# Performance work log

Measured on AMD Instinct MI355X. Metric: run time of the kernel, lower is better.

## Reference

```python
import jax, jax.numpy as jnp
import numpy as np


def setup_inputs() -> dict:
    key = jax.random.key(0)
    ks = jax.random.split(key, 6)
    B, C, H, W = 8, 1024, 48, 48
    K = 32            # keep_topk
    Cg = C // K       # channels per group = 32
    return {
        "corr_features": jax.random.normal(ks[0], (B, H, W, H, W), jnp.float32),
        "cur_features": jax.random.normal(ks[1], (B, C, H, W), jnp.float32),
        "ref_mask": jax.random.uniform(ks[2], (B, 1, 384, 384), dtype=jnp.float32),
        # grouped 1x1 conv: per-group weight [K, out_per_group, in_per_group]
        "group_w": jax.random.normal(ks[3], (K, Cg, Cg), jnp.float32) * 0.02,
        "group_b": jnp.zeros((C,), jnp.float32),
        # global 1x1 conv: [out=Cg, in=C]
        "global_w": jax.random.normal(ks[4], (Cg, C), jnp.float32) * 0.02,
        "global_b": jnp.zeros((Cg,), jnp.float32),
    }


def reference(corr_features, cur_features, ref_mask, group_w, group_b, global_w, global_b):
    B, ch, cw, rh, rw = corr_features.shape
    C = cur_features.shape[1]
    K, Cg, _ = group_w.shape  # K = keep_topk, Cg = C // K

    cur_flat = cur_features.reshape(B, C, ch * cw)          # [B,C,N]
    corr = corr_features.reshape(B, ch * cw, rh * rw)       # [B,N,M]

    # F.interpolate(..., mode='bilinear', align_corners=False) == half-pixel linear resize
    mask = jax.image.resize(ref_mask, (B, 1, rh, rw), method="linear")
    mask = (mask.reshape(B, 1, rh * rw) > 0.5).astype(jnp.float32)
    fg_corr = corr * mask                                    # [B,N,M]

    # get_struct_info: topk over summed correlation, gather channel features
    scores = fg_corr.sum(axis=-1)                            # [B,N]
    _, idx = jax.lax.top_k(scores, K)                        # [B,K]
    struct = jnp.take_along_axis(cur_flat, idx[:, None, :], axis=2)  # [B,C,K]
    struct = jnp.swapaxes(struct, 1, 2)                      # [B,K,C]

    # bmm(struct, cur_flat): [B,K,C] x [B,C,N] -> [B,K,N]
    struct_info = jnp.einsum('bkc,bcn->bkn', struct, cur_flat).reshape(B, K, ch, cw)

    # grouped 1x1 conv (groups=K) + ReLU
    xg = cur_features.reshape(B, K, Cg, ch, cw)
    group_feat = jnp.einsum('bkihw,koi->bkohw', xg, group_w)
    group_feat = jax.nn.relu(group_feat + group_b.reshape(K, Cg)[None, :, :, None, None])

    # repeat struct_info across each group's Cg channels, multiply, sum over groups
    group_struct = (struct_info[:, :, None, :, :] * group_feat).sum(axis=1)  # [B,Cg,H,W]

    # global 1x1 conv + ReLU
    global_feat = jnp.einsum('bchw,oc->bohw', cur_features, global_w)
    global_feat = jax.nn.relu(global_feat + global_b[None, :, None, None])   # [B,Cg,H,W]
    global_struct = struct_info.mean(axis=1, keepdims=True) * global_feat

    return jnp.concatenate([group_struct, global_struct], axis=1)  # [B,2*Cg,H,W]
```

## Files before the change

### kernel.cpp

```cpp
#include <hip/hip_runtime.h>
#include <math.h>

#define BB 8
#define CC 1024
#define HW 48
#define NN 2304
#define MM 2304
#define KK 32

typedef __attribute__((ext_vector_type(8))) short short8v;
typedef __attribute__((ext_vector_type(4))) float f32x4;

__device__ __forceinline__ unsigned short f2bf(float f) {
    unsigned u = __float_as_uint(f);
    return (unsigned short)((u + 0x7FFFu + ((u >> 16) & 1u)) >> 16);
}

__device__ __forceinline__ void gll16(const unsigned short* g, unsigned short* l) {
    __builtin_amdgcn_global_load_lds(
        (const __attribute__((address_space(1))) void*)g,
        (__attribute__((address_space(3))) void*)l, 16, 0, 0);
}

__global__ void mask_kernel(const float* __restrict__ rm, float* __restrict__ mask) {
    int t = blockIdx.x * 256 + threadIdx.x;
    if (t >= BB * NN) return;
    int b = t / NN, p = t % NN;
    int y = p / HW, x = p % HW;
    const float* src = rm + (size_t)b * 384 * 384;

    int jx0 = 8 * x - 4;
    float wx[16];
    float wxs = 0.f;
    #pragma unroll
    for (int dx = 0; dx < 16; ++dx) {
        int jx = jx0 + dx;
        float w = 1.0f - fabsf((float)dx - 7.5f) * 0.125f;
        if (jx >= 0 && jx < 384) { wx[dx] = w; wxs += w; } else wx[dx] = 0.f;
    }
    int jy0 = 8 * y - 4;
    float acc = 0.f, wys = 0.f;
    for (int dy = 0; dy < 16; ++dy) {
        int jy = jy0 + dy;
        if (jy < 0 || jy >= 384) continue;
        float wy = 1.0f - fabsf((float)dy - 7.5f) * 0.125f;
        wys += wy;
        const float* row = src + (size_t)jy * 384;
        float rs = 0.f;
        #pragma unroll
        for (int dx = 0; dx < 16; ++dx) {
            if (wx[dx] > 0.f) rs += wx[dx] * row[jx0 + dx];
        }
        acc += wy * rs;
    }
    float v = acc / (wys * wxs);
    mask[t] = (v > 0.5f) ? 1.0f : 0.0f;
}

__global__ void scores_kernel(const float* __restrict__ corr, const float* __restrict__ mask,
                              float* __restrict__ scores) {
    int wave = threadIdx.x >> 6, lane = threadIdx.x & 63;
    int row = blockIdx.x * 4 + wave;
    int b = row / NN, n = row % NN;
    const float4* cr = (const float4*)(corr + ((size_t)b * NN + n) * MM);
    const float4* mr = (const float4*)(mask + (size_t)b * MM);
    float acc = 0.f;
    #pragma unroll
    for (int it = 0; it < 9; ++it) {
        int i = it * 64 + lane;
        float4 cv = cr[i];
        float4 mv = mr[i];
        acc += cv.x * mv.x + cv.y * mv.y + cv.z * mv.z + cv.w * mv.w;
    }
    #pragma unroll
    for (int off = 32; off >= 1; off >>= 1) acc += __shfl_down(acc, off);
    if (lane == 0) scores[row] = acc;
}

__global__ void topk1_kernel(const float* __restrict__ scores,
                             float* __restrict__ cval, int* __restrict__ cidx) {
    int b = blockIdx.x >> 3, ch = blockIdx.x & 7;
    int t = threadIdx.x;
    const float* s = scores + b * NN + ch * 288;
    float v0 = s[t];
    float v1 = (t < 32) ? s[256 + t] : -INFINITY;
    int i0 = t, i1 = 256 + t;
    __shared__ float wv[4]; __shared__ int wi[4];
    __shared__ float bwv; __shared__ int bwi;
    for (int it = 0; it < KK; ++it) {
        float bv = (v0 >= v1) ? v0 : v1;
        int   bi = (v0 >= v1) ? i0 : i1;
        #pragma unroll
        for (int off = 32; off >= 1; off >>= 1) {
            float ov = __shfl_down(bv, off);
            int   oi = __shfl_down(bi, off);
            if (ov > bv || (ov == bv && oi < bi)) { bv = ov; bi = oi; }
        }
        if ((t & 63) == 0) { wv[t >> 6] = bv; wi[t >> 6] = bi; }
        __syncthreads();
        if (t == 0) {
            #pragma unroll
            for (int u = 1; u < 4; ++u)
                if (wv[u] > bv || (wv[u] == bv && wi[u] < bi)) { bv = wv[u]; bi = wi[u]; }
            bwv = bv; bwi = bi;
            cval[(b * 8 + ch) * 32 + it] = bv;
            cidx[(b * 8 + ch) * 32 + it] = ch * 288 + bi;
        }
        __syncthreads();
        int W = bwi;
        if (i0 == W) v0 = -INFINITY;
        if (i1 == W) v1 = -INFINITY;
    }
}

__global__ void topk2_kernel(const float* __restrict__ cval, const int* __restrict__ cidx,
                             int* __restrict__ idxo) {
    int b = blockIdx.x, t = threadIdx.x;
    float v = cval[b * 256 + t];
    int gi = cidx[b * 256 + t];
    __shared__ float wv[4]; __shared__ int wi[4];
    __shared__ int bwi_s;
    for (int it = 0; it < KK; ++it) {
        float bv = v; int bi = gi;
        #pragma unroll
        for (int off = 32; off >= 1; off >>= 1) {
            float ov = __shfl_down(bv, off);
            int   oi = __shfl_down(bi, off);
            if (ov > bv || (ov == bv && oi < bi)) { bv = ov; bi = oi; }
        }
        if ((t & 63) == 0) { wv[t >> 6] = bv; wi[t >> 6] = bi; }
        __syncthreads();
        if (t == 0) {
            #pragma unroll
            for (int u = 1; u < 4; ++u)
                if (wv[u] > bv || (wv[u] == bv && wi[u] < bi)) { bv = wv[u]; bi = wi[u]; }
            idxo[b * KK + it] = bi;
            bwi_s = bi;
        }
        __syncthreads();
        if (gi == bwi_s) v = -INFINITY;
    }
}

__global__ void gather_kernel(const float* __restrict__ cur, const int* __restrict__ idx,
                              unsigned short* __restrict__ st) {
    int t = blockIdx.x * 256 + threadIdx.x;
    int c = t & (CC - 1); int bk = t >> 10; int k = bk & 31; int b = bk >> 5;
    int id = idx[b * KK + k];
    st[t] = f2bf(cur[((size_t)b * CC + c) * NN + id]);
}

__global__ void wconv_kernel(const float* __restrict__ gw, const float* __restrict__ glw,
                             unsigned short* __restrict__ gwh, unsigned short* __restrict__ glwh) {
    int t = blockIdx.x * 256 + threadIdx.x;
    gwh[t] = f2bf(gw[t]);
    glwh[t] = f2bf(glw[t]);
}

__global__ __launch_bounds__(256) void fused_mfma(
    const float* __restrict__ cur, const unsigned short* __restrict__ st16,
    const unsigned short* __restrict__ gwh, const unsigned short* __restrict__ glwh,
    const float* __restrict__ gb, const float* __restrict__ glb,
    float* __restrict__ out)
{
    __shared__ unsigned short XT[2][1024];
    __shared__ unsigned short AC[2][1024];
    __shared__ unsigned short GC[2][1024];
    __shared__ float SIL[32][33];
    __shared__ float GBL[CC];
    __shared__ float MS[32];
    __shared__ float GLBL[32];

    int blk = blockIdx.x;
    int b = blk / 72, n0 = (blk % 72) * 32;
    int t = threadIdx.x;
    int w = t >> 6, l = t & 63;
    int m = w >> 1, nt = w & 1;

    for (int i = t; i < CC; i += 256) GBL[i] = gb[i];
    if (t < 32) GLBL[t] = glb[t];

    const float* curb = cur + (size_t)b * CC * NN;
    const unsigned short* stb = st16 + b * (KK * CC);

    int ci = t >> 3, ns = t & 7;
    const float* xsrc0 = curb + (size_t)(2 * ci) * NN + n0 + 4 * ns;
    const float* xsrc1 = xsrc0 + NN;

    int fro = (16 * m + (l & 15)) * 32 + 8 * (l >> 4);
    int fxo = (16 * nt + (l & 15)) * 32 + 8 * (l >> 4);

    if (t < 128) {
        float4 f0 = *(const float4*)(xsrc0);
        float4 f1 = *(const float4*)(xsrc1);
        unsigned pk;
        pk = (unsigned)f2bf(f0.x) | ((unsigned)f2bf(f1.x) << 16); *(unsigned*)&XT[0][(4*ns+0)*32 + 2*ci] = pk;
        pk = (unsigned)f2bf(f0.y) | ((unsigned)f2bf(f1.y) << 16); *(unsigned*)&XT[0][(4*ns+1)*32 + 2*ci] = pk;
        pk = (unsigned)f2bf(f0.z) | ((unsigned)f2bf(f1.z) << 16); *(unsigned*)&XT[0][(4*ns+2)*32 + 2*ci] = pk;
        pk = (unsigned)f2bf(f0.w) | ((unsigned)f2bf(f1.w) << 16); *(unsigned*)&XT[0][(4*ns+3)*32 + 2*ci] = pk;
    } else if (w == 2) {
        gll16(stb + (l >> 2) * CC + (l & 3) * 8, &AC[0][0]);
        gll16(stb + (16 + (l >> 2)) * CC + (l & 3) * 8, &AC[0][512]);
    } else {
        gll16(glwh + (l >> 2) * CC + (l & 3) * 8, &GC[0][0]);
        gll16(glwh + (16 + (l >> 2)) * CC + (l & 3) * 8, &GC[0][512]);
    }
    __syncthreads();

    f32x4 siacc = {0.f, 0.f, 0.f, 0.f};
    f32x4 glacc = {0.f, 0.f, 0.f, 0.f};
    for (int cc = 0; cc < 32; ++cc) {
        int buf = cc & 1;
        bool stg = (cc < 31);
        float4 f0, f1;
        if (stg) {
            if (t < 128) {
                f0 = *(const float4*)(xsrc0 + (size_t)(cc + 1) * 32 * NN);
                f1 = *(const float4*)(xsrc1 + (size_t)(cc + 1) * 32 * NN);
            } else if (w == 2) {
                gll16(stb + (l >> 2) * CC + (cc + 1) * 32 + (l & 3) * 8, &AC[buf ^ 1][0]);
                gll16(stb + (16 + (l >> 2)) * CC + (cc + 1) * 32 + (l & 3) * 8, &AC[buf ^ 1][512]);
            } else {
                gll16(glwh + (l >> 2) * CC + (cc + 1) * 32 + (l & 3) * 8, &GC[buf ^ 1][0]);
                gll16(glwh + (16 + (l >> 2)) * CC + (cc + 1) * 32 + (l & 3) * 8, &GC[buf ^ 1][512]);
            }
        }
        short8v ast = *(const short8v*)&AC[buf][fro];
        short8v agl = *(const short8v*)&GC[buf][fro];
        short8v bx  = *(const short8v*)&XT[buf][fxo];
        siacc = __builtin_amdgcn_mfma_f32_16x16x32_bf16(ast, bx, siacc, 0, 0, 0);
        glacc = __builtin_amdgcn_mfma_f32_16x16x32_bf16(agl, bx, glacc, 0, 0, 0);
        if (stg && t < 128) {
            int bo = buf ^ 1;
            unsigned pk;
            pk = (unsigned)f2bf(f0.x) | ((unsigned)f2bf(f1.x) << 16); *(unsigned*)&XT[bo][(4*ns+0)*32 + 2*ci] = pk;
            pk = (unsigned)f2bf(f0.y) | ((unsigned)f2bf(f1.y) << 16); *(unsigned*)&XT[bo][(4*ns+1)*32 + 2*ci] = pk;
            pk = (unsigned)f2bf(f0.z) | ((unsigned)f2bf(f1.z) << 16); *(unsigned*)&XT[bo][(4*ns+2)*32 + 2*ci] = pk;
            pk = (unsigned)f2bf(f0.w) | ((unsigned)f2bf(f1.w) << 16); *(unsigned*)&XT[bo][(4*ns+3)*32 + 2*ci] = pk;
        }
        __syncthreads();
    }

    #pragma unroll
    for (int r = 0; r < 4; ++r)
        SIL[16 * m + 4 * (l >> 4) + r][16 * nt + (l & 15)] = siacc[r];
    __syncthreads();
    if (t < 32) {
        float s = 0.f;
        #pragma unroll
        for (int k = 0; k < 32; ++k) s += SIL[k][t];
        MS[t] = s * (1.0f / 32.0f);
    }

    if (t < 128) {
        float4 f0 = *(const float4*)(xsrc0);
        float4 f1 = *(const float4*)(xsrc1);
        unsigned pk;
        pk = (unsigned)f2bf(f0.x) | ((unsigned)f2bf(f1.x) << 16); *(unsigned*)&XT[0][(4*ns+0)*32 + 2*ci] = pk;
        pk = (unsigned)f2bf(f0.y) | ((unsigned)f2bf(f1.y) << 16); *(unsigned*)&XT[0][(4*ns+1)*32 + 2*ci] = pk;
        pk = (unsigned)f2bf(f0.z) | ((unsigned)f2bf(f1.z) << 16); *(unsigned*)&XT[0][(4*ns+2)*32 + 2*ci] = pk;
        pk = (unsigned)f2bf(f0.w) | ((unsigned)f2bf(f1.w) << 16); *(unsigned*)&XT[0][(4*ns+3)*32 + 2*ci] = pk;
    } else if (w == 2) {
        gll16(gwh + l * 8, &AC[0][0]);
        gll16(gwh + 512 + l * 8, &AC[0][512]);
    }
    __syncthreads();

    f32x4 accg = {0.f, 0.f, 0.f, 0.f};
    const f32x4 zz = {0.f, 0.f, 0.f, 0.f};
    for (int k = 0; k < 32; ++k) {
        int buf = k & 1;
        bool stg = (k < 31);
        float4 f0, f1;
        if (stg) {
            if (t < 128) {
                f0 = *(const float4*)(xsrc0 + (size_t)(k + 1) * 32 * NN);
                f1 = *(const float4*)(xsrc1 + (size_t)(k + 1) * 32 * NN);
            } else if (w == 2) {
                gll16(gwh + (k + 1) * 1024 + l * 8, &AC[buf ^ 1][0]);
                gll16(gwh + (k + 1) * 1024 + 512 + l * 8, &AC[buf ^ 1][512]);
            }
        }
        short8v aw = *(const short8v*)&AC[buf][fro];
        short8v bx = *(const short8v*)&XT[buf][fxo];
        f32x4 gf = __builtin_amdgcn_mfma_f32_16x16x32_bf16(aw, bx, zz, 0, 0, 0);
        float sik = SIL[k][16 * nt + (l & 15)];
        #pragma unroll
        for (int r = 0; r < 4; ++r) {
            int orow = 16 * m + 4 * (l >> 4) + r;
            accg[r] += sik * fmaxf(gf[r] + GBL[k * 32 + orow], 0.f);
        }
        if (stg && t < 128) {
            int bo = buf ^ 1;
            unsigned pk;
            pk = (unsigned)f2bf(f0.x) | ((unsigned)f2bf(f1.x) << 16); *(unsigned*)&XT[bo][(4*ns+0)*32 + 2*ci] = pk;
            pk = (unsigned)f2bf(f0.y) | ((unsigned)f2bf(f1.y) << 16); *(unsigned*)&XT[bo][(4*ns+1)*32 + 2*ci] = pk;
            pk = (unsigned)f2bf(f0.z) | ((unsigned)f2bf(f1.z) << 16); *(unsigned*)&XT[bo][(4*ns+2)*32 + 2*ci] = pk;
            pk = (unsigned)f2bf(f0.w) | ((unsigned)f2bf(f1.w) << 16); *(unsigned*)&XT[bo][(4*ns+3)*32 + 2*ci] = pk;
        }
        __syncthreads();
    }

    int col = 16 * nt + (l & 15);
    size_t ob = (size_t)b * 64 * NN + n0 + col;
    float msv = MS[col];
    #pragma unroll
    for (int r = 0; r < 4; ++r) {
        int orow = 16 * m + 4 * (l >> 4) + r;
        out[ob + (size_t)orow * NN] = accg[r];
        out[ob + (size_t)(32 + orow) * NN] = fmaxf(glacc[r] + GLBL[orow], 0.f) * msv;
    }
}

extern "C" void kernel_launch(void* const* d_in, const int* in_sizes, int n_in,
                              void* d_out, int out_size, void* d_ws, size_t ws_size,
                              hipStream_t stream) {
    const float* corr = (const float*)d_in[0];
    const float* cur  = (const float*)d_in[1];
    const float* rm   = (const float*)d_in[2];
    const float* gw   = (const float*)d_in[3];
    const float* gb   = (const float*)d_in[4];
    const float* glw  = (const float*)d_in[5];
    const float* glb  = (const float*)d_in[6];
    float* out = (float*)d_out;
    float* ws  = (float*)d_ws;

    float* mask   = ws;
    float* scores = mask + BB * MM;
    float* cval   = scores + BB * NN;
    int*   cidx   = (int*)(cval + 2048);
    int*   idx    = cidx + 2048;
    unsigned short* st16 = (unsigned short*)(idx + 256);
    unsigned short* gwh  = st16 + BB * KK * CC;
    unsigned short* glwh = gwh + 32768;

    mask_kernel<<<(BB * NN + 255) / 256, 256, 0, stream>>>(rm, mask);
    scores_kernel<<<BB * NN / 4, 256, 0, stream>>>(corr, mask, scores);
    topk1_kernel<<<BB * 8, 256, 0, stream>>>(scores, cval, cidx);
    topk2_kernel<<<BB, 256, 0, stream>>>(cval, cidx, idx);
    gather_kernel<<<BB * KK * CC / 256, 256, 0, stream>>>(cur, idx, st16);
    wconv_kernel<<<128, 256, 0, stream>>>(gw, glw, gwh, glwh);
    fused_mfma<<<BB * (NN / 32), 256, 0, stream>>>(cur, st16, gwh, glwh, gb, glb, out);
}
```

Measured before the change: 172.7 us.

## Stage full-channel X tile once in LDS and split group conv across waves

The fused MFMA kernel now uses 16-column tiles instead of 32 and loads all 1024 channels of the current-feature tile into LDS once, as bf16 with an XOR swizzle. This replaces the two separate streamed, double-buffered passes over the same data, which had a barrier on every step. The A operands (struct rows, global weights, group weights) are read straight from global memory, not staged through LDS. Each wave now covers 8 of the 32 groups, and the partial sums are reduced through LDS at the end. The grid doubles and LDS use grows to about 32KB per block, which may limit occupancy.

```diff
diff --git a/kernel.cpp b/kernel.cpp
--- a/kernel.cpp
+++ b/kernel.cpp
@@ -14,12 +14,6 @@
 __device__ __forceinline__ unsigned short f2bf(float f) {
     unsigned u = __float_as_uint(f);
     return (unsigned short)((u + 0x7FFFu + ((u >> 16) & 1u)) >> 16);
-}
-
-__device__ __forceinline__ void gll16(const unsigned short* g, unsigned short* l) {
-    __builtin_amdgcn_global_load_lds(
-        (const __attribute__((address_space(1))) void*)g,
-        (__attribute__((address_space(3))) void*)l, 16, 0, 0);
 }
 
 __global__ void mask_kernel(const float* __restrict__ rm, float* __restrict__ mask) {
@@ -86,7 +80,7 @@
     float v1 = (t < 32) ? s[256 + t] : -INFINITY;
     int i0 = t, i1 = 256 + t;
     __shared__ float wv[4]; __shared__ int wi[4];
-    __shared__ float bwv; __shared__ int bwi;
+    __shared__ int bwi;
     for (int it = 0; it < KK; ++it) {
         float bv = (v0 >= v1) ? v0 : v1;
         int   bi = (v0 >= v1) ? i0 : i1;
@@ -102,7 +96,7 @@
             #pragma unroll
             for (int u = 1; u < 4; ++u)
                 if (wv[u] > bv || (wv[u] == bv && wi[u] < bi)) { bv = wv[u]; bi = wi[u]; }
-            bwv = bv; bwi = bi;
+            bwi = bi;
             cval[(b * 8 + ch) * 32 + it] = bv;
             cidx[(b * 8 + ch) * 32 + it] = ch * 288 + bi;
         }
@@ -163,152 +157,106 @@
     const float* __restrict__ gb, const float* __restrict__ glb,
     float* __restrict__ out)
 {
-    __shared__ unsigned short XT[2][1024];
-    __shared__ unsigned short AC[2][1024];
-    __shared__ unsigned short GC[2][1024];
-    __shared__ float SIL[32][33];
+    __shared__ unsigned short XT[16 * 1024];
+    __shared__ float SIL[32][18];
+    __shared__ float PART[4][2][256];
+    __shared__ float MS[16];
     __shared__ float GBL[CC];
-    __shared__ float MS[32];
     __shared__ float GLBL[32];
 
-    int blk = blockIdx.x;
-    int b = blk / 72, n0 = (blk % 72) * 32;
+    int hw = blockIdx.x;
+    int b = hw & 7;
+    int n0 = (hw >> 3) * 16;
     int t = threadIdx.x;
     int w = t >> 6, l = t & 63;
-    int m = w >> 1, nt = w & 1;
+    int mrow = w & 1, mat = w >> 1;
+    int nrow = l & 15, kq = l >> 4;
 
     for (int i = t; i < CC; i += 256) GBL[i] = gb[i];
     if (t < 32) GLBL[t] = glb[t];
 
     const float* curb = cur + (size_t)b * CC * NN;
-    const unsigned short* stb = st16 + b * (KK * CC);
-
-    int ci = t >> 3, ns = t & 7;
-    const float* xsrc0 = curb + (size_t)(2 * ci) * NN + n0 + 4 * ns;
-    const float* xsrc1 = xsrc0 + NN;
-
-    int fro = (16 * m + (l & 15)) * 32 + 8 * (l >> 4);
-    int fxo = (16 * nt + (l & 15)) * 32 + 8 * (l >> 4);
-
-    if (t < 128) {
-        float4 f0 = *(const float4*)(xsrc0);
-        float4 f1 = *(const float4*)(xsrc1);
-        unsigned pk;
-        pk = (unsigned)f2bf(f0.x) | ((unsigned)f2bf(f1.x) << 16); *(unsigned*)&XT[0][(4*ns+0)*32 + 2*ci] = pk;
-        pk = (unsigned)f2bf(f0.y) | ((unsigned)f2bf(f1.y) << 16); *(unsigned*)&XT[0][(4*ns+1)*32 + 2*ci] = pk;
-        pk = (unsigned)f2bf(f0.z) | ((unsigned)f2bf(f1.z) << 16); *(unsigned*)&XT[0][(4*ns+2)*32 + 2*ci] = pk;
-        pk = (unsigned)f2bf(f0.w) | ((unsigned)f2bf(f1.w) << 16); *(unsigned*)&XT[0][(4*ns+3)*32 + 2*ci] = pk;
-    } else if (w == 2) {
-        gll16(stb + (l >> 2) * CC + (l & 3) * 8, &AC[0][0]);
-        gll16(stb + (16 + (l >> 2)) * CC + (l & 3) * 8, &AC[0][512]);
-    } else {
-        gll16(glwh + (l >> 2) * CC + (l & 3) * 8, &GC[0][0]);
-        gll16(glwh + (16 + (l >> 2)) * CC + (l & 3) * 8, &GC[0][512]);
+    int nq = t & 3, ci0 = t >> 2;
+    #pragma unroll
+    for (int q = 0; q < 8; ++q) {
+        int ci = ci0 + 64 * q;
+        int c = 2 * ci;
+        const float* p0 = curb + (size_t)c * NN + n0 + 4 * nq;
+        float4 f0 = *(const float4*)p0;
+        float4 f1 = *(const float4*)(p0 + NN);
+        float a0[4] = {f0.x, f0.y, f0.z, f0.w};
+        float a1[4] = {f1.x, f1.y, f1.z, f1.w};
+        #pragma unroll
+        for (int r = 0; r < 4; ++r) {
+            int n = 4 * nq + r;
+            unsigned pk = (unsigned)f2bf(a0[r]) | ((unsigned)f2bf(a1[r]) << 16);
+            *(unsigned*)((char*)XT + n * 2048 + ((((ci >> 2) ^ (n & 7)) << 4) + ((ci & 3) << 2))) = pk;
+        }
     }
     __syncthreads();
 
-    f32x4 siacc = {0.f, 0.f, 0.f, 0.f};
-    f32x4 glacc = {0.f, 0.f, 0.f, 0.f};
+    const char* xbase = (const char*)XT + nrow * 2048;
+    const unsigned short* Abase = (mat == 0 ? st16 + (size_t)b * KK * CC : glwh)
+                                  + (size_t)(16 * mrow + nrow) * CC + 8 * kq;
+    f32x4 acc = {0.f, 0.f, 0.f, 0.f};
+    #pragma unroll 8
     for (int cc = 0; cc < 32; ++cc) {
-        int buf = cc & 1;
-        bool stg = (cc < 31);
-        float4 f0, f1;
-        if (stg) {
-            if (t < 128) {
-                f0 = *(const float4*)(xsrc0 + (size_t)(cc + 1) * 32 * NN);
-                f1 = *(const float4*)(xsrc1 + (size_t)(cc + 1) * 32 * NN);
-            } else if (w == 2) {
-                gll16(stb + (l >> 2) * CC + (cc + 1) * 32 + (l & 3) * 8, &AC[buf ^ 1][0]);
-                gll16(stb + (16 + (l >> 2)) * CC + (cc + 1) * 32 + (l & 3) * 8, &AC[buf ^ 1][512]);
-            } else {
-                gll16(glwh + (l >> 2) * CC + (cc + 1) * 32 + (l & 3) * 8, &GC[buf ^ 1][0]);
-                gll16(glwh + (16 + (l >> 2)) * CC + (cc + 1) * 32 + (l & 3) * 8, &GC[buf ^ 1][512]);
-            }
-        }
-        short8v ast = *(const short8v*)&AC[buf][fro];
-        short8v agl = *(const short8v*)&GC[buf][fro];
-        short8v bx  = *(const short8v*)&XT[buf][fxo];
-        siacc = __builtin_amdgcn_mfma_f32_16x16x32_bf16(ast, bx, siacc, 0, 0, 0);
-        glacc = __builtin_amdgcn_mfma_f32_16x16x32_bf16(agl, bx, glacc, 0, 0, 0);
-        if (stg && t < 128) {
-            int bo = buf ^ 1;
-            unsigned pk;
-            pk = (unsigned)f2bf(f0.x) | ((unsigned)f2bf(f1.x) << 16); *(unsigned*)&XT[bo][(4*ns+0)*32 + 2*ci] = pk;
-            pk = (unsigned)f2bf(f0.y) | ((unsigned)f2bf(f1.y) << 16); *(unsigned*)&XT[bo][(4*ns+1)*32 + 2*ci] = pk;
-            pk = (unsigned)f2bf(f0.z) | ((unsigned)f2bf(f1.z) << 16); *(unsigned*)&XT[bo][(4*ns+2)*32 + 2*ci] = pk;
-            pk = (unsigned)f2bf(f0.w) | ((unsigned)f2bf(f1.w) << 16); *(unsigned*)&XT[bo][(4*ns+3)*32 + 2*ci] = pk;
-        }
-        __syncthreads();
-    }
-
-    #pragma unroll
-    for (int r = 0; r < 4; ++r)
-        SIL[16 * m + 4 * (l >> 4) + r][16 * nt + (l & 15)] = siacc[r];
+        short8v A = *(const short8v*)(Abase + cc * 32);
+        short8v B = *(const short8v*)(xbase + (((cc * 4 + kq) ^ (nrow & 7)) << 4));
+        acc = __builtin_amdgcn_mfma_f32_16x16x32_bf16(A, B, acc, 0, 0, 0);
+    }
+
+    if (mat == 0) {
+        #pragma unroll
+        for (int r = 0; r < 4; ++r)
+            SIL[16 * mrow + 4 * kq + r][nrow] = acc[r];
+    }
     __syncthreads();
-    if (t < 32) {
+    if (t < 16) {
         float s = 0.f;
         #pragma unroll
         for (int k = 0; k < 32; ++k) s += SIL[k][t];
         MS[t] = s * (1.0f / 32.0f);
     }
 
-    if (t < 128) {
-        float4 f0 = *(const float4*)(xsrc0);
-        float4 f1 = *(const float4*)(xsrc1);
-        unsigned pk;
-        pk = (unsigned)f2bf(f0.x) | ((unsigned)f2bf(f1.x) << 16); *(unsigned*)&XT[0][(4*ns+0)*32 + 2*ci] = pk;
-        pk = (unsigned)f2bf(f0.y) | ((unsigned)f2bf(f1.y) << 16); *(unsigned*)&XT[0][(4*ns+1)*32 + 2*ci] = pk;
-        pk = (unsigned)f2bf(f0.z) | ((unsigned)f2bf(f1.z) << 16); *(unsigned*)&XT[0][(4*ns+2)*32 + 2*ci] = pk;
-        pk = (unsigned)f2bf(f0.w) | ((unsigned)f2bf(f1.w) << 16); *(unsigned*)&XT[0][(4*ns+3)*32 + 2*ci] = pk;
-    } else if (w == 2) {
-        gll16(gwh + l * 8, &AC[0][0]);
-        gll16(gwh + 512 + l * 8, &AC[0][512]);
-    }
+    f32x4 p0 = {0.f, 0.f, 0.f, 0.f}, p1 = {0.f, 0.f, 0.f, 0.f};
+    const f32x4 zz = {0.f, 0.f, 0.f, 0.f};
+    #pragma unroll
+    for (int j = 0; j < 8; ++j) {
+        int k = 8 * w + j;
+        const unsigned short* gk = gwh + k * 1024 + 8 * kq;
+        short8v A0 = *(const short8v*)(gk + nrow * 32);
+        short8v A1 = *(const short8v*)(gk + (16 + nrow) * 32);
+        short8v B = *(const short8v*)(xbase + (((k * 4 + kq) ^ (nrow & 7)) << 4));
+        f32x4 g0 = __builtin_amdgcn_mfma_f32_16x16x32_bf16(A0, B, zz, 0, 0, 0);
+        f32x4 g1 = __builtin_amdgcn_mfma_f32_16x16x32_bf16(A1, B, zz, 0, 0, 0);
+        float sik = SIL[k][nrow];
+        #pragma unroll
+        for (int r = 0; r < 4; ++r) {
+            p0[r] += sik * fmaxf(g0[r] + GBL[k * 32 + 4 * kq + r], 0.f);
+            p1[r] += sik * fmaxf(g1[r] + GBL[k * 32 + 16 + 4 * kq + r], 0.f);
+        }
+    }
+    *(f32x4*)&PART[w][0][l * 4] = p0;
+    *(f32x4*)&PART[w][1][l * 4] = p1;
     __syncthreads();
 
-    f32x4 accg = {0.f, 0.f, 0.f, 0.f};
-    const f32x4 zz = {0.f, 0.f, 0.f, 0.f};
-    for (int k = 0; k < 32; ++k) {
-        int buf = k & 1;
-        bool stg = (k < 31);
-        float4 f0, f1;
-        if (stg) {
-            if (t < 128) {
-                f0 = *(const float4*)(xsrc0 + (size_t)(k + 1) * 32 * NN);
-                f1 = *(const float4*)(xsrc1 + (size_t)(k + 1) * 32 * NN);
-            } else if (w == 2) {
-                gll16(gwh + (k + 1) * 1024 + l * 8, &AC[buf ^ 1][0]);
-                gll16(gwh + (k + 1) * 1024 + 512 + l * 8, &AC[buf ^ 1][512]);
-            }
-        }
-        short8v aw = *(const short8v*)&AC[buf][fro];
-        short8v bx = *(const short8v*)&XT[buf][fxo];
-        f32x4 gf = __builtin_amdgcn_mfma_f32_16x16x32_bf16(aw, bx, zz, 0, 0, 0);
-        float sik = SIL[k][16 * nt + (l & 15)];
-        #pragma unroll
-        for (int r = 0; r < 4; ++r) {
-            int orow = 16 * m + 4 * (l >> 4) + r;
-            accg[r] += sik * fmaxf(gf[r] + GBL[k * 32 + orow], 0.f);
-        }
-        if (stg && t < 128) {
-            int bo = buf ^ 1;
-            unsigned pk;
-            pk = (unsigned)f2bf(f0.x) | ((unsigned)f2bf(f1.x) << 16); *(unsigned*)&XT[bo][(4*ns+0)*32 + 2*ci] = pk;
-            pk = (unsigned)f2bf(f0.y) | ((unsigned)f2bf(f1.y) << 16); *(unsigned*)&XT[bo][(4*ns+1)*32 + 2*ci] = pk;
-            pk = (unsigned)f2bf(f0.z) | ((unsigned)f2bf(f1.z) << 16); *(unsigned*)&XT[bo][(4*ns+2)*32 + 2*ci] = pk;
-            pk = (unsigned)f2bf(f0.w) | ((unsigned)f2bf(f1.w) << 16); *(unsigned*)&XT[bo][(4*ns+3)*32 + 2*ci] = pk;
-        }
-        __syncthreads();
-    }
-
-    int col = 16 * nt + (l & 15);
-    size_t ob = (size_t)b * 64 * NN + n0 + col;
-    float msv = MS[col];
-    #pragma unroll
-    for (int r = 0; r < 4; ++r) {
-        int orow = 16 * m + 4 * (l >> 4) + r;
-        out[ob + (size_t)orow * NN] = accg[r];
-        out[ob + (size_t)(32 + orow) * NN] = fmaxf(glacc[r] + GLBL[orow], 0.f) * msv;
+    size_t ob = (size_t)b * 64 * NN + n0 + nrow;
+    if (mat == 0) {
+        #pragma unroll
+        for (int r = 0; r < 4; ++r) {
+            int li = l * 4 + r;
+            float v = PART[0][mrow][li] + PART[1][mrow][li]
+                    + PART[2][mrow][li] + PART[3][mrow][li];
+            out[ob + (size_t)(16 * mrow + 4 * kq + r) * NN] = v;
+        }
+    } else {
+        float msv = MS[nrow];
+        #pragma unroll
+        for (int r = 0; r < 4; ++r) {
+            int o = 16 * mrow + 4 * kq + r;
+            out[ob + (size_t)(32 + o) * NN] = fmaxf(acc[r] + GLBL[o], 0.f) * msv;
+        }
     }
 }
 
@@ -340,5 +288,5 @@
     topk2_kernel<<<BB, 256, 0, stream>>>(cval, cidx, idx);
     gather_kernel<<<BB * KK * CC / 256, 256, 0, stream>>>(cur, idx, st16);
     wconv_kernel<<<128, 256, 0, stream>>>(gw, glw, gwh, glwh);
-    fused_mfma<<<BB * (NN / 32), 256, 0, stream>>>(cur, st16, gwh, glwh, gb, glb, out);
-}
+    fused_mfma<<<BB * (NN / 16), 256, 0, stream>>>(cur, st16, gwh, glwh, gb, glb, out);
+}
```

Result: faster. 165.0 us (-4.5%).
